# Performance work log

Hardware: AMD Instinct MI355X
Metric: run time of the kernel (lower is better)

The kernel has to match this reference:

```python
import jax, jax.numpy as jnp
import numpy as np

N = 100000
E = 1600000
D_IN = 64
HIDDEN = [64, 64]
D_OUT = 64


def _sage_layer(x, src, dst, Wl, bl, Wr):
    # gather source features, scatter-max into destination nodes
    agg = jax.ops.segment_max(x[src], dst, num_segments=x.shape[0])  # [N, d_in]
    agg = jnp.where(jnp.isfinite(agg), agg, jnp.zeros((), x.dtype))  # isolated nodes -> 0 (PyG fill)
    return agg @ Wl + bl + x @ Wr  # lin_l(aggr) + lin_r(x), bias only on lin_l


def setup_inputs() -> dict:
    key = jax.random.key(0)
    ks = jax.random.split(key, 12)
    x = jax.random.normal(ks[0], (N, D_IN), dtype=jnp.float32)
    edge_index = jax.random.randint(ks[1], (2, E), 0, N, dtype=jnp.int64)
    dims = [D_IN] + HIDDEN + [D_OUT]  # [64, 64, 64, 64]
    inp = {"x": x, "edge_index": edge_index}
    for i in range(3):
        din, dout = dims[i], dims[i + 1]
        s = 1.0 / np.sqrt(din)
        inp[f"Wl{i}"] = jax.random.uniform(ks[2 + 3 * i], (din, dout), jnp.float32, -s, s)
        inp[f"bl{i}"] = jax.random.uniform(ks[3 + 3 * i], (dout,), jnp.float32, -s, s)
        inp[f"Wr{i}"] = jax.random.uniform(ks[4 + 3 * i], (din, dout), jnp.float32, -s, s)
    return inp


def reference(x, edge_index, Wl0, bl0, Wr0, Wl1, bl1, Wr1, Wl2, bl2, Wr2):
    src, dst = edge_index[0], edge_index[1]
    # dropout p=0.0 -> identity; relu after every conv including the last
    h = jax.nn.relu(_sage_layer(x, src, dst, Wl0, bl0, Wr0))
    h = jax.nn.relu(_sage_layer(h, src, dst, Wl1, bl1, Wr1))
    h = jax.nn.relu(_sage_layer(h, src, dst, Wl2, bl2, Wr2))
    return h
```

## Files before the change

### kernel.cpp

```cpp
#include <hip/hip_runtime.h>
#include <math.h>

#define THREADS 256
#define CHUNK 4096
#define SLAB 4096

typedef __attribute__((ext_vector_type(8))) short bf16x8;
typedef __attribute__((ext_vector_type(4))) float f32x4;

__device__ __forceinline__ float bf_lo(unsigned w) { return __uint_as_float(w << 16); }
__device__ __forceinline__ float bf_hi(unsigned w) { return __uint_as_float(w & 0xffff0000u); }
__device__ __forceinline__ unsigned rne(float f) {
    unsigned b = __float_as_uint(f);
    return b + 0x7fffu + ((b >> 16) & 1u);
}

__device__ __forceinline__ int detect64(const int* __restrict__ ei) {
    return ((ei[1] | ei[3] | ei[5] | ei[7] | ei[9] | ei[11]) == 0) ? 1 : 0;
}
__device__ __forceinline__ int get_src(const int* ei, int e, int i, int is64) {
    return is64 ? (int)((const long long*)ei)[i] : ei[i];
}
__device__ __forceinline__ int get_dst(const int* ei, int e, int i, int is64) {
    return is64 ? (int)((const long long*)ei)[e + i] : ei[e + i];
}

__global__ void k_zero_int(int* __restrict__ p, int n) {
    int i = blockIdx.x * blockDim.x + threadIdx.x;
    if (i < n) p[i] = 0;
}

__global__ __launch_bounds__(256) void k_cvtw(const float4* __restrict__ x4, uint2* __restrict__ hb, int n4,
                                              const float* __restrict__ Wl0, const float* __restrict__ Wr0,
                                              const float* __restrict__ Wl1, const float* __restrict__ Wr1,
                                              const float* __restrict__ Wl2, const float* __restrict__ Wr2,
                                              unsigned* __restrict__ wt0, unsigned* __restrict__ wt1,
                                              unsigned* __restrict__ wt2) {
    int i = blockIdx.x * 256 + threadIdx.x;
    if (i < n4) {
        float4 v = x4[i];
        unsigned p0 = (rne(v.x) >> 16) | (rne(v.y) & 0xffff0000u);
        unsigned p1 = (rne(v.z) >> 16) | (rne(v.w) & 0xffff0000u);
        hb[i] = make_uint2(p0, p1);
        return;
    }
    int id = i - n4;
    if (id < 3 * 4096) {
        int layer = id >> 12;
        int r = id & 4095;
        const float* Wl = (layer == 0) ? Wl0 : (layer == 1) ? Wl1 : Wl2;
        const float* Wr = (layer == 0) ? Wr0 : (layer == 1) ? Wr1 : Wr2;
        unsigned* wt = (layer == 0) ? wt0 : (layer == 1) ? wt1 : wt2;
        int nrow = r >> 6;
        int k2 = r & 63;
        const float* W = (k2 < 32) ? Wl : Wr;
        int k = (k2 < 32) ? (k2 * 2) : (k2 * 2 - 64);
        unsigned lo = rne(W[k * 64 + nrow]) >> 16;
        unsigned hi = rne(W[(k + 1) * 64 + nrow]) & 0xffff0000u;
        wt[nrow * 64 + k2] = lo | hi;
    }
}


__global__ __launch_bounds__(256) void k_bscatter(const int* __restrict__ ei, int e,
                                                  int* __restrict__ bucket_cur,
                                                  int* __restrict__ part, int nbuckets) {
    __shared__ int hist[1024];
    __shared__ int basev[1024];
    int t = threadIdx.x;
#pragma unroll
    for (int j = 0; j < 4; j++) hist[t + j * 256] = 0;
    __syncthreads();
    int is64 = detect64(ei);
    int base = blockIdx.x * CHUNK;
    int ds[16], ss[16];
#pragma unroll
    for (int it = 0; it < 16; it++) {
        int i = base + t + it * 256;
        ds[it] = -1;
        ss[it] = 0;
        if (i < e) {
            ds[it] = get_dst(ei, e, i, is64);
            ss[it] = get_src(ei, e, i, is64);
            atomicAdd(&hist[ds[it] >> 7], 1);
        }
    }
    __syncthreads();
#pragma unroll
    for (int j = 0; j < 4; j++) {
        int b = t + j * 256;
        if (b < nbuckets) {
            int c = hist[b];
            if (c) basev[b] = atomicAdd(&bucket_cur[b], c);
        }
    }
    __syncthreads();
#pragma unroll
    for (int it = 0; it < 16; it++) {
        if (ds[it] >= 0) {
            int bk = ds[it] >> 7;
            int pos = atomicAdd(&basev[bk], 1);
            pos = min(pos, SLAB - 1);
            part[bk * SLAB + pos] = (ss[it] << 7) | (ds[it] & 127);
        }
    }
}

__global__ __launch_bounds__(1024) void k_bscan(const int* __restrict__ bucket_cnt, int nbuckets,
                                                int* __restrict__ bucket_ptr,
                                                int* __restrict__ row_ptr, int n, int e) {
    __shared__ int s[1024];
    int t = threadIdx.x;
    int v = (t < nbuckets) ? bucket_cnt[t] : 0;
    s[t] = v;
    __syncthreads();
    for (int off = 1; off < 1024; off <<= 1) {
        int u = (t >= off) ? s[t - off] : 0;
        __syncthreads();
        s[t] += u;
        __syncthreads();
    }
    if (t < nbuckets) bucket_ptr[t] = s[t] - v;
    if (t == 0) {
        bucket_ptr[nbuckets] = e;
        row_ptr[n] = e;
    }
}

__global__ __launch_bounds__(256) void k_bfinal(const int* __restrict__ part,
                                                const int* __restrict__ bucket_ptr,
                                                int* __restrict__ row_ptr,
                                                int* __restrict__ col, int n) {
    __shared__ int deg[128], cur[128], sc[128];
    int b = blockIdx.x, t = threadIdx.x;
    int beg = bucket_ptr[b], end = bucket_ptr[b + 1];
    int cnt = end - beg;
    const int* slab = part + b * SLAB;
    int node0 = b << 7;
    if (t < 128) deg[t] = 0;
    __syncthreads();
    for (int i = t; i < cnt; i += 256) atomicAdd(&deg[slab[i] & 127], 1);
    __syncthreads();
    int v = (t < 128) ? deg[t] : 0;
    if (t < 128) sc[t] = v;
    __syncthreads();
    for (int off = 1; off < 128; off <<= 1) {
        int u = (t < 128 && t >= off) ? sc[t - off] : 0;
        __syncthreads();
        if (t < 128) sc[t] += u;
        __syncthreads();
    }
    if (t < 128) {
        int ex = beg + sc[t] - v;
        if (node0 + t < n) row_ptr[node0 + t] = ex;
        cur[t] = ex;
    }
    __syncthreads();
    for (int i = t; i < cnt; i += 256) {
        int p = slab[i];
        int pos = atomicAdd(&cur[p & 127], 1);
        col[pos] = p >> 7;
    }
}

__global__ __launch_bounds__(512, 8) void k_fused(const unsigned* __restrict__ hin,
                                                  const int* __restrict__ row_ptr,
                                                  const int* __restrict__ col,
                                                  const unsigned* __restrict__ Wt,
                                                  const float* __restrict__ bl,
                                                  float* __restrict__ outf,
                                                  unsigned* __restrict__ outb,
                                                  int n) {
    __shared__ char smem[17408 + 17408 + 256];
    short (*Abuf)[136] = (short(*)[136])smem;
    float (*Cs)[68] = (float(*)[68])smem;
    short (*Wts)[136] = (short(*)[136])(smem + 17408);
    float* bs = (float*)(smem + 34816);

    int t = threadIdx.x;
    int node0 = blockIdx.x * 64;

#pragma unroll
    for (int it = 0; it < 2; it++) {
        int c = t + it * 512;
        int nr = c >> 4, k16 = c & 15;
        uint4 w = *(const uint4*)(Wt + nr * 64 + k16 * 4);
        *(uint4*)&Wts[nr][k16 * 8] = w;
    }
    {
        int row = t >> 3, k8 = t & 7;
        int node = node0 + row;
        uint4 w = make_uint4(0, 0, 0, 0);
        if (node < n) w = *(const uint4*)(hin + (size_t)node * 32 + k8 * 4);
        *(uint4*)&Abuf[row][64 + k8 * 8] = w;
    }
    if (t < 64) bs[t] = bl[t];

    int off = (t & 15) << 1;
#pragma unroll
    for (int pass = 0; pass < 2; pass++) {
        int gl = pass * 32 + (t >> 4);
        int g = node0 + gl;
        float4 m = make_float4(0.f, 0.f, 0.f, 0.f);
        if (g < n) {
            int b = row_ptr[g], e = row_ptr[g + 1];
            if (b < e) {
                m = make_float4(-INFINITY, -INFINITY, -INFINITY, -INFINITY);
                int e1 = e - 1;
                for (int k = b; k < e; k += 16) {
                    int s0 = col[min(k, e1)];
                    int s1 = col[min(k + 1, e1)];
                    int s2 = col[min(k + 2, e1)];
                    int s3 = col[min(k + 3, e1)];
                    int s4 = col[min(k + 4, e1)];
                    int s5 = col[min(k + 5, e1)];
                    int s6 = col[min(k + 6, e1)];
                    int s7 = col[min(k + 7, e1)];
                    uint2 r0 = *(const uint2*)(hin + (unsigned)(s0 * 32 + off));
                    uint2 r1 = *(const uint2*)(hin + (unsigned)(s1 * 32 + off));
                    uint2 r2 = *(const uint2*)(hin + (unsigned)(s2 * 32 + off));
                    uint2 r3 = *(const uint2*)(hin + (unsigned)(s3 * 32 + off));
                    uint2 r4 = *(const uint2*)(hin + (unsigned)(s4 * 32 + off));
                    uint2 r5 = *(const uint2*)(hin + (unsigned)(s5 * 32 + off));
                    uint2 r6 = *(const uint2*)(hin + (unsigned)(s6 * 32 + off));
                    uint2 r7 = *(const uint2*)(hin + (unsigned)(s7 * 32 + off));
                    int u0 = col[min(k + 8, e1)];
                    int u1 = col[min(k + 9, e1)];
                    int u2 = col[min(k + 10, e1)];
                    int u3 = col[min(k + 11, e1)];
                    int u4 = col[min(k + 12, e1)];
                    int u5 = col[min(k + 13, e1)];
                    int u6 = col[min(k + 14, e1)];
                    int u7 = col[min(k + 15, e1)];
                    uint2 q0 = *(const uint2*)(hin + (unsigned)(u0 * 32 + off));
                    uint2 q1 = *(const uint2*)(hin + (unsigned)(u1 * 32 + off));
                    uint2 q2 = *(const uint2*)(hin + (unsigned)(u2 * 32 + off));
                    uint2 q3 = *(const uint2*)(hin + (unsigned)(u3 * 32 + off));
                    uint2 q4 = *(const uint2*)(hin + (unsigned)(u4 * 32 + off));
                    uint2 q5 = *(const uint2*)(hin + (unsigned)(u5 * 32 + off));
                    uint2 q6 = *(const uint2*)(hin + (unsigned)(u6 * 32 + off));
                    uint2 q7 = *(const uint2*)(hin + (unsigned)(u7 * 32 + off));
                    m.x = fmaxf(m.x, fmaxf(fmaxf(fmaxf(bf_lo(r0.x), bf_lo(r1.x)), fmaxf(bf_lo(r2.x), bf_lo(r3.x))),
                                           fmaxf(fmaxf(bf_lo(r4.x), bf_lo(r5.x)), fmaxf(bf_lo(r6.x), bf_lo(r7.x)))));
                    m.y = fmaxf(m.y, fmaxf(fmaxf(fmaxf(bf_hi(r0.x), bf_hi(r1.x)), fmaxf(bf_hi(r2.x), bf_hi(r3.x))),
                                           fmaxf(fmaxf(bf_hi(r4.x), bf_hi(r5.x)), fmaxf(bf_hi(r6.x), bf_hi(r7.x)))));
                    m.z = fmaxf(m.z, fmaxf(fmaxf(fmaxf(bf_lo(r0.y), bf_lo(r1.y)), fmaxf(bf_lo(r2.y), bf_lo(r3.y))),
                                           fmaxf(fmaxf(bf_lo(r4.y), bf_lo(r5.y)), fmaxf(bf_lo(r6.y), bf_lo(r7.y)))));
                    m.w = fmaxf(m.w, fmaxf(fmaxf(fmaxf(bf_hi(r0.y), bf_hi(r1.y)), fmaxf(bf_hi(r2.y), bf_hi(r3.y))),
                                           fmaxf(fmaxf(bf_hi(r4.y), bf_hi(r5.y)), fmaxf(bf_hi(r6.y), bf_hi(r7.y)))));
                    m.x = fmaxf(m.x, fmaxf(fmaxf(fmaxf(bf_lo(q0.x), bf_lo(q1.x)), fmaxf(bf_lo(q2.x), bf_lo(q3.x))),
                                           fmaxf(fmaxf(bf_lo(q4.x), bf_lo(q5.x)), fmaxf(bf_lo(q6.x), bf_lo(q7.x)))));
                    m.y = fmaxf(m.y, fmaxf(fmaxf(fmaxf(bf_hi(q0.x), bf_hi(q1.x)), fmaxf(bf_hi(q2.x), bf_hi(q3.x))),
                                           fmaxf(fmaxf(bf_hi(q4.x), bf_hi(q5.x)), fmaxf(bf_hi(q6.x), bf_hi(q7.x)))));
                    m.z = fmaxf(m.z, fmaxf(fmaxf(fmaxf(bf_lo(q0.y), bf_lo(q1.y)), fmaxf(bf_lo(q2.y), bf_lo(q3.y))),
                                           fmaxf(fmaxf(bf_lo(q4.y), bf_lo(q5.y)), fmaxf(bf_lo(q6.y), bf_lo(q7.y)))));
                    m.w = fmaxf(m.w, fmaxf(fmaxf(fmaxf(bf_hi(q0.y), bf_hi(q1.y)), fmaxf(bf_hi(q2.y), bf_hi(q3.y))),
                                           fmaxf(fmaxf(bf_hi(q4.y), bf_hi(q5.y)), fmaxf(bf_hi(q6.y), bf_hi(q7.y)))));
                }
            }
        }
        unsigned p0 = (__float_as_uint(m.x) >> 16) | (__float_as_uint(m.y) & 0xffff0000u);
        unsigned p1 = (__float_as_uint(m.z) >> 16) | (__float_as_uint(m.w) & 0xffff0000u);
        *(uint2*)&Abuf[gl][(t & 15) * 4] = make_uint2(p0, p1);
    }
    __syncthreads();

    int lane = t & 63;
    int wv = t >> 6;
    int r0 = (wv & 3) * 16;
    int c0 = (wv >> 2) * 32;
    int lr = lane & 15, lk = lane >> 4;

    f32x4 acc0 = {0.f, 0.f, 0.f, 0.f}, acc1 = acc0;
#pragma unroll
    for (int kk = 0; kk < 4; kk++) {
        int ko = kk * 32 + lk * 8;
        bf16x8 a = *(const bf16x8*)&Abuf[r0 + lr][ko];
        bf16x8 b0 = *(const bf16x8*)&Wts[c0 + lr][ko];
        bf16x8 b1 = *(const bf16x8*)&Wts[c0 + 16 + lr][ko];
        acc0 = __builtin_amdgcn_mfma_f32_16x16x32_bf16(a, b0, acc0, 0, 0, 0);
        acc1 = __builtin_amdgcn_mfma_f32_16x16x32_bf16(a, b1, acc1, 0, 0, 0);
    }
    __syncthreads();
#pragma unroll
    for (int reg = 0; reg < 4; reg++) {
        int row = r0 + lk * 4 + reg;
        Cs[row][c0 + lr] = acc0[reg];
        Cs[row][c0 + 16 + lr] = acc1[reg];
    }
    __syncthreads();

#pragma unroll
    for (int it = 0; it < 2; it++) {
        int idx = t + it * 512;
        int row = idx >> 4, qc = idx & 15;
        int node = node0 + row;
        if (node < n) {
            float4 v = *(float4*)&Cs[row][qc * 4];
            float4 bb = *(float4*)&bs[qc * 4];
            float4 o;
            o.x = fmaxf(v.x + bb.x, 0.f);
            o.y = fmaxf(v.y + bb.y, 0.f);
            o.z = fmaxf(v.z + bb.z, 0.f);
            o.w = fmaxf(v.w + bb.w, 0.f);
            if (outf) *(float4*)(outf + (size_t)node * 64 + qc * 4) = o;
            if (outb) {
                unsigned p0 = (rne(o.x) >> 16) | (rne(o.y) & 0xffff0000u);
                unsigned p1 = (rne(o.z) >> 16) | (rne(o.w) & 0xffff0000u);
                *(uint2*)(outb + (size_t)node * 32 + qc * 2) = make_uint2(p0, p1);
            }
        }
    }
}


extern "C" void kernel_launch(void* const* d_in, const int* in_sizes, int n_in,
                              void* d_out, int out_size, void* d_ws, size_t ws_size,
                              hipStream_t stream) {
    const float* x = (const float*)d_in[0];
    const int* ei = (const int*)d_in[1];
    const float* Wl0 = (const float*)d_in[2];
    const float* bl0 = (const float*)d_in[3];
    const float* Wr0 = (const float*)d_in[4];
    const float* Wl1 = (const float*)d_in[5];
    const float* bl1 = (const float*)d_in[6];
    const float* Wr1 = (const float*)d_in[7];
    const float* Wl2 = (const float*)d_in[8];
    const float* bl2 = (const float*)d_in[9];
    const float* Wr2 = (const float*)d_in[10];

    int n = in_sizes[0] / 64;
    int e = in_sizes[1] / 2;
    int nbuckets = (n + 127) >> 7;

    char* p = (char*)d_ws;
    auto alloc = [&](size_t bytes) {
        void* q = (void*)p;
        p += (bytes + 255) & ~(size_t)255;
        return q;
    };
    int* bucket_cur = (int*)alloc((size_t)nbuckets * 4);
    int* bucket_ptr = (int*)alloc(((size_t)nbuckets + 1) * 4);
    int* row_ptr = (int*)alloc(((size_t)n + 1) * 4);
    int* col = (int*)alloc((size_t)e * 4);
    int* part = (int*)alloc((size_t)nbuckets * SLAB * 4);
    unsigned* hb0 = (unsigned*)alloc((size_t)n * 64 * 2);
    unsigned* hb1 = (unsigned*)alloc((size_t)n * 64 * 2);
    unsigned* wt0 = (unsigned*)alloc(64 * 64 * 4);
    unsigned* wt1 = (unsigned*)alloc(64 * 64 * 4);
    unsigned* wt2 = (unsigned*)alloc(64 * 64 * 4);

    float* out = (float*)d_out;

    int gb_chunk = (e + CHUNK - 1) / CHUNK;
    int gb_fused = (n + 63) / 64;
    int n4 = n * 16;
    int gb_cvtw = (n4 + 3 * 4096 + THREADS - 1) / THREADS;

    k_zero_int<<<(nbuckets + THREADS - 1) / THREADS, THREADS, 0, stream>>>(bucket_cur, nbuckets);
    k_bscatter<<<gb_chunk, 256, 0, stream>>>(ei, e, bucket_cur, part, nbuckets);
    k_bscan<<<1, 1024, 0, stream>>>(bucket_cur, nbuckets, bucket_ptr, row_ptr, n, e);
    k_bfinal<<<nbuckets, 256, 0, stream>>>(part, bucket_ptr, row_ptr, col, n);

    k_cvtw<<<gb_cvtw, THREADS, 0, stream>>>((const float4*)x, (uint2*)hb0, n4,
                                            Wl0, Wr0, Wl1, Wr1, Wl2, Wr2, wt0, wt1, wt2);

    k_fused<<<gb_fused, 512, 0, stream>>>(hb0, row_ptr, col, wt0, bl0, (float*)nullptr, hb1, n);
    k_fused<<<gb_fused, 512, 0, stream>>>(hb1, row_ptr, col, wt1, bl1, (float*)nullptr, hb0, n);
    k_fused<<<gb_fused, 512, 0, stream>>>(hb0, row_ptr, col, wt2, bl2, out, (unsigned*)nullptr, n);
}
```

Before: 176.1 us.

## Use order-preserving bf16 encoding with packed u16 max and padded slab CSR

Stores bf16 features in a monotone unsigned encoding so the segment max can use packed v_pk_max_u16 instead of unpacking to fp32 and calling fmaxf. The CSR is rebuilt per bucket slab with each node's degree padded to a multiple of 8 (padding repeats the first neighbour) and column entries pre-scaled to byte offsets, which allows aligned int4 column loads without clamping. The global bucket scan kernel is removed, and row_beg/row_end arrays replace row_ptr. The cost is extra encode/decode work, padded gathers on low-degree nodes, and a larger col buffer.

Result: faster. 157.1 us (-10.8%).

```diff
diff --git a/kernel.cpp b/kernel.cpp
--- a/kernel.cpp
+++ b/kernel.cpp
@@ -8,11 +8,23 @@
 typedef __attribute__((ext_vector_type(8))) short bf16x8;
 typedef __attribute__((ext_vector_type(4))) float f32x4;
 
-__device__ __forceinline__ float bf_lo(unsigned w) { return __uint_as_float(w << 16); }
-__device__ __forceinline__ float bf_hi(unsigned w) { return __uint_as_float(w & 0xffff0000u); }
 __device__ __forceinline__ unsigned rne(float f) {
     unsigned b = __float_as_uint(f);
     return b + 0x7fffu + ((b >> 16) & 1u);
+}
+
+__device__ __forceinline__ unsigned enc_map(unsigned u) {
+    return u ^ (((((u >> 15) & 0x00010001u) * 0xFFFFu)) | 0x80008000u);
+}
+__device__ __forceinline__ unsigned dec_map(unsigned e) {
+    return e ^ ((((((~e) >> 15) & 0x00010001u) * 0xFFFFu)) | 0x80008000u);
+}
+#define ENC_NEG_INF 0x007F007Fu
+
+__device__ __forceinline__ unsigned pkmax(unsigned a, unsigned b) {
+    unsigned d;
+    asm("v_pk_max_u16 %0, %1, %2" : "=v"(d) : "v"(a), "v"(b));
+    return d;
 }
 
 __device__ __forceinline__ int detect64(const int* __restrict__ ei) {
@@ -41,7 +53,7 @@
         float4 v = x4[i];
         unsigned p0 = (rne(v.x) >> 16) | (rne(v.y) & 0xffff0000u);
         unsigned p1 = (rne(v.z) >> 16) | (rne(v.w) & 0xffff0000u);
-        hb[i] = make_uint2(p0, p1);
+        hb[i] = make_uint2(enc_map(p0), enc_map(p1));
         return;
     }
     int id = i - n4;
@@ -106,35 +118,14 @@
     }
 }
 
-__global__ __launch_bounds__(1024) void k_bscan(const int* __restrict__ bucket_cnt, int nbuckets,
-                                                int* __restrict__ bucket_ptr,
-                                                int* __restrict__ row_ptr, int n, int e) {
-    __shared__ int s[1024];
-    int t = threadIdx.x;
-    int v = (t < nbuckets) ? bucket_cnt[t] : 0;
-    s[t] = v;
-    __syncthreads();
-    for (int off = 1; off < 1024; off <<= 1) {
-        int u = (t >= off) ? s[t - off] : 0;
-        __syncthreads();
-        s[t] += u;
-        __syncthreads();
-    }
-    if (t < nbuckets) bucket_ptr[t] = s[t] - v;
-    if (t == 0) {
-        bucket_ptr[nbuckets] = e;
-        row_ptr[n] = e;
-    }
-}
-
 __global__ __launch_bounds__(256) void k_bfinal(const int* __restrict__ part,
-                                                const int* __restrict__ bucket_ptr,
-                                                int* __restrict__ row_ptr,
+                                                const int* __restrict__ bucket_cnt,
+                                                int* __restrict__ row_beg,
+                                                int* __restrict__ row_end,
                                                 int* __restrict__ col, int n) {
     __shared__ int deg[128], cur[128], sc[128];
     int b = blockIdx.x, t = threadIdx.x;
-    int beg = bucket_ptr[b], end = bucket_ptr[b + 1];
-    int cnt = end - beg;
+    int cnt = bucket_cnt[b];
     const int* slab = part + b * SLAB;
     int node0 = b << 7;
     if (t < 128) deg[t] = 0;
@@ -142,7 +133,8 @@
     for (int i = t; i < cnt; i += 256) atomicAdd(&deg[slab[i] & 127], 1);
     __syncthreads();
     int v = (t < 128) ? deg[t] : 0;
-    if (t < 128) sc[t] = v;
+    int dp = (v > 0) ? ((v + 7) & ~7) : 0;
+    if (t < 128) sc[t] = dp;
     __syncthreads();
     for (int off = 1; off < 128; off <<= 1) {
         int u = (t < 128 && t >= off) ? sc[t - off] : 0;
@@ -150,21 +142,33 @@
         if (t < 128) sc[t] += u;
         __syncthreads();
     }
+    int base = b * SLAB;
+    int beg = 0;
     if (t < 128) {
-        int ex = beg + sc[t] - v;
-        if (node0 + t < n) row_ptr[node0 + t] = ex;
-        cur[t] = ex;
+        beg = base + sc[t] - dp;
+        int node = node0 + t;
+        if (node < n) {
+            row_beg[node] = beg;
+            row_end[node] = beg + dp;
+        }
+        cur[t] = beg;
     }
     __syncthreads();
     for (int i = t; i < cnt; i += 256) {
         int p = slab[i];
         int pos = atomicAdd(&cur[p & 127], 1);
-        col[pos] = p >> 7;
+        col[pos] = p & ~127;
+    }
+    __syncthreads();
+    if (t < 128 && v > 0) {
+        int first = col[beg];
+        for (int j = v; j < dp; j++) col[beg + j] = first;
     }
 }
 
 __global__ __launch_bounds__(512, 8) void k_fused(const unsigned* __restrict__ hin,
-                                                  const int* __restrict__ row_ptr,
+                                                  const int* __restrict__ row_beg,
+                                                  const int* __restrict__ row_end,
                                                   const int* __restrict__ col,
                                                   const unsigned* __restrict__ Wt,
                                                   const float* __restrict__ bl,
@@ -191,77 +195,50 @@
         int row = t >> 3, k8 = t & 7;
         int node = node0 + row;
         uint4 w = make_uint4(0, 0, 0, 0);
-        if (node < n) w = *(const uint4*)(hin + (size_t)node * 32 + k8 * 4);
+        if (node < n) {
+            w = *(const uint4*)(hin + (size_t)node * 32 + k8 * 4);
+            w.x = dec_map(w.x);
+            w.y = dec_map(w.y);
+            w.z = dec_map(w.z);
+            w.w = dec_map(w.w);
+        }
         *(uint4*)&Abuf[row][64 + k8 * 8] = w;
     }
     if (t < 64) bs[t] = bl[t];
 
-    int off = (t & 15) << 1;
+    const char* hp = (const char*)hin;
+    int off8 = (t & 15) << 3;
 #pragma unroll
     for (int pass = 0; pass < 2; pass++) {
         int gl = pass * 32 + (t >> 4);
         int g = node0 + gl;
-        float4 m = make_float4(0.f, 0.f, 0.f, 0.f);
+        uint2 res = make_uint2(0u, 0u);
         if (g < n) {
-            int b = row_ptr[g], e = row_ptr[g + 1];
+            int b = row_beg[g], e = row_end[g];
             if (b < e) {
-                m = make_float4(-INFINITY, -INFINITY, -INFINITY, -INFINITY);
-                int e1 = e - 1;
-                for (int k = b; k < e; k += 16) {
-                    int s0 = col[min(k, e1)];
-                    int s1 = col[min(k + 1, e1)];
-                    int s2 = col[min(k + 2, e1)];
-                    int s3 = col[min(k + 3, e1)];
-                    int s4 = col[min(k + 4, e1)];
-                    int s5 = col[min(k + 5, e1)];
-                    int s6 = col[min(k + 6, e1)];
-                    int s7 = col[min(k + 7, e1)];
-                    uint2 r0 = *(const uint2*)(hin + (unsigned)(s0 * 32 + off));
-                    uint2 r1 = *(const uint2*)(hin + (unsigned)(s1 * 32 + off));
-                    uint2 r2 = *(const uint2*)(hin + (unsigned)(s2 * 32 + off));
-                    uint2 r3 = *(const uint2*)(hin + (unsigned)(s3 * 32 + off));
-                    uint2 r4 = *(const uint2*)(hin + (unsigned)(s4 * 32 + off));
-                    uint2 r5 = *(const uint2*)(hin + (unsigned)(s5 * 32 + off));
-                    uint2 r6 = *(const uint2*)(hin + (unsigned)(s6 * 32 + off));
-                    uint2 r7 = *(const uint2*)(hin + (unsigned)(s7 * 32 + off));
-                    int u0 = col[min(k + 8, e1)];
-                    int u1 = col[min(k + 9, e1)];
-                    int u2 = col[min(k + 10, e1)];
-                    int u3 = col[min(k + 11, e1)];
-                    int u4 = col[min(k + 12, e1)];
-                    int u5 = col[min(k + 13, e1)];
-                    int u6 = col[min(k + 14, e1)];
-                    int u7 = col[min(k + 15, e1)];
-                    uint2 q0 = *(const uint2*)(hin + (unsigned)(u0 * 32 + off));
-                    uint2 q1 = *(const uint2*)(hin + (unsigned)(u1 * 32 + off));
-                    uint2 q2 = *(const uint2*)(hin + (unsigned)(u2 * 32 + off));
-                    uint2 q3 = *(const uint2*)(hin + (unsigned)(u3 * 32 + off));
-                    uint2 q4 = *(const uint2*)(hin + (unsigned)(u4 * 32 + off));
-                    uint2 q5 = *(const uint2*)(hin + (unsigned)(u5 * 32 + off));
-                    uint2 q6 = *(const uint2*)(hin + (unsigned)(u6 * 32 + off));
-                    uint2 q7 = *(const uint2*)(hin + (unsigned)(u7 * 32 + off));
-                    m.x = fmaxf(m.x, fmaxf(fmaxf(fmaxf(bf_lo(r0.x), bf_lo(r1.x)), fmaxf(bf_lo(r2.x), bf_lo(r3.x))),
-                                           fmaxf(fmaxf(bf_lo(r4.x), bf_lo(r5.x)), fmaxf(bf_lo(r6.x), bf_lo(r7.x)))));
-                    m.y = fmaxf(m.y, fmaxf(fmaxf(fmaxf(bf_hi(r0.x), bf_hi(r1.x)), fmaxf(bf_hi(r2.x), bf_hi(r3.x))),
-                                           fmaxf(fmaxf(bf_hi(r4.x), bf_hi(r5.x)), fmaxf(bf_hi(r6.x), bf_hi(r7.x)))));
-                    m.z = fmaxf(m.z, fmaxf(fmaxf(fmaxf(bf_lo(r0.y), bf_lo(r1.y)), fmaxf(bf_lo(r2.y), bf_lo(r3.y))),
-                                           fmaxf(fmaxf(bf_lo(r4.y), bf_lo(r5.y)), fmaxf(bf_lo(r6.y), bf_lo(r7.y)))));
-                    m.w = fmaxf(m.w, fmaxf(fmaxf(fmaxf(bf_hi(r0.y), bf_hi(r1.y)), fmaxf(bf_hi(r2.y), bf_hi(r3.y))),
-                                           fmaxf(fmaxf(bf_hi(r4.y), bf_hi(r5.y)), fmaxf(bf_hi(r6.y), bf_hi(r7.y)))));
-                    m.x = fmaxf(m.x, fmaxf(fmaxf(fmaxf(bf_lo(q0.x), bf_lo(q1.x)), fmaxf(bf_lo(q2.x), bf_lo(q3.x))),
-                                           fmaxf(fmaxf(bf_lo(q4.x), bf_lo(q5.x)), fmaxf(bf_lo(q6.x), bf_lo(q7.x)))));
-                    m.y = fmaxf(m.y, fmaxf(fmaxf(fmaxf(bf_hi(q0.x), bf_hi(q1.x)), fmaxf(bf_hi(q2.x), bf_hi(q3.x))),
-                                           fmaxf(fmaxf(bf_hi(q4.x), bf_hi(q5.x)), fmaxf(bf_hi(q6.x), bf_hi(q7.x)))));
-                    m.z = fmaxf(m.z, fmaxf(fmaxf(fmaxf(bf_lo(q0.y), bf_lo(q1.y)), fmaxf(bf_lo(q2.y), bf_lo(q3.y))),
-                                           fmaxf(fmaxf(bf_lo(q4.y), bf_lo(q5.y)), fmaxf(bf_lo(q6.y), bf_lo(q7.y)))));
-                    m.w = fmaxf(m.w, fmaxf(fmaxf(fmaxf(bf_hi(q0.y), bf_hi(q1.y)), fmaxf(bf_hi(q2.y), bf_hi(q3.y))),
-                                           fmaxf(fmaxf(bf_hi(q4.y), bf_hi(q5.y)), fmaxf(bf_hi(q6.y), bf_hi(q7.y)))));
+                unsigned m0 = ENC_NEG_INF, m1 = ENC_NEG_INF;
+                for (int k = b; k < e; k += 8) {
+                    int4 c0 = *(const int4*)(col + k);
+                    int4 c1 = *(const int4*)(col + k + 4);
+                    uint2 r0 = *(const uint2*)(hp + (unsigned)(c0.x + off8));
+                    uint2 r1 = *(const uint2*)(hp + (unsigned)(c0.y + off8));
+                    uint2 r2 = *(const uint2*)(hp + (unsigned)(c0.z + off8));
+                    uint2 r3 = *(const uint2*)(hp + (unsigned)(c0.w + off8));
+                    uint2 r4 = *(const uint2*)(hp + (unsigned)(c1.x + off8));
+                    uint2 r5 = *(const uint2*)(hp + (unsigned)(c1.y + off8));
+                    uint2 r6 = *(const uint2*)(hp + (unsigned)(c1.z + off8));
+                    uint2 r7 = *(const uint2*)(hp + (unsigned)(c1.w + off8));
+                    unsigned a0 = pkmax(pkmax(r0.x, r1.x), pkmax(r2.x, r3.x));
+                    unsigned a1 = pkmax(pkmax(r4.x, r5.x), pkmax(r6.x, r7.x));
+                    unsigned b0 = pkmax(pkmax(r0.y, r1.y), pkmax(r2.y, r3.y));
+                    unsigned b1 = pkmax(pkmax(r4.y, r5.y), pkmax(r6.y, r7.y));
+                    m0 = pkmax(m0, pkmax(a0, a1));
+                    m1 = pkmax(m1, pkmax(b0, b1));
                 }
+                res = make_uint2(dec_map(m0), dec_map(m1));
             }
         }
-        unsigned p0 = (__float_as_uint(m.x) >> 16) | (__float_as_uint(m.y) & 0xffff0000u);
-        unsigned p1 = (__float_as_uint(m.z) >> 16) | (__float_as_uint(m.w) & 0xffff0000u);
-        *(uint2*)&Abuf[gl][(t & 15) * 4] = make_uint2(p0, p1);
+        *(uint2*)&Abuf[gl][(t & 15) * 4] = res;
     }
     __syncthreads();
 
@@ -307,7 +284,7 @@
             if (outb) {
                 unsigned p0 = (rne(o.x) >> 16) | (rne(o.y) & 0xffff0000u);
                 unsigned p1 = (rne(o.z) >> 16) | (rne(o.w) & 0xffff0000u);
-                *(uint2*)(outb + (size_t)node * 32 + qc * 2) = make_uint2(p0, p1);
+                *(uint2*)(outb + (size_t)node * 32 + qc * 2) = make_uint2(enc_map(p0), enc_map(p1));
             }
         }
     }
@@ -340,9 +317,9 @@
         return q;
     };
     int* bucket_cur = (int*)alloc((size_t)nbuckets * 4);
-    int* bucket_ptr = (int*)alloc(((size_t)nbuckets + 1) * 4);
-    int* row_ptr = (int*)alloc(((size_t)n + 1) * 4);
-    int* col = (int*)alloc((size_t)e * 4);
+    int* row_beg = (int*)alloc((size_t)n * 4);
+    int* row_end = (int*)alloc((size_t)n * 4);
+    int* col = (int*)alloc((size_t)nbuckets * SLAB * 4);
     int* part = (int*)alloc((size_t)nbuckets * SLAB * 4);
     unsigned* hb0 = (unsigned*)alloc((size_t)n * 64 * 2);
     unsigned* hb1 = (unsigned*)alloc((size_t)n * 64 * 2);
@@ -359,13 +336,12 @@
 
     k_zero_int<<<(nbuckets + THREADS - 1) / THREADS, THREADS, 0, stream>>>(bucket_cur, nbuckets);
     k_bscatter<<<gb_chunk, 256, 0, stream>>>(ei, e, bucket_cur, part, nbuckets);
-    k_bscan<<<1, 1024, 0, stream>>>(bucket_cur, nbuckets, bucket_ptr, row_ptr, n, e);
-    k_bfinal<<<nbuckets, 256, 0, stream>>>(part, bucket_ptr, row_ptr, col, n);
+    k_bfinal<<<nbuckets, 256, 0, stream>>>(part, bucket_cur, row_beg, row_end, col, n);
 
     k_cvtw<<<gb_cvtw, THREADS, 0, stream>>>((const float4*)x, (uint2*)hb0, n4,
                                             Wl0, Wr0, Wl1, Wr1, Wl2, Wr2, wt0, wt1, wt2);
 
-    k_fused<<<gb_fused, 512, 0, stream>>>(hb0, row_ptr, col, wt0, bl0, (float*)nullptr, hb1, n);
-    k_fused<<<gb_fused, 512, 0, stream>>>(hb1, row_ptr, col, wt1, bl1, (float*)nullptr, hb0, n);
-    k_fused<<<gb_fused, 512, 0, stream>>>(hb0, row_ptr, col, wt2, bl2, out, (unsigned*)nullptr, n);
-}
+    k_fused<<<gb_fused, 512, 0, stream>>>(hb0, row_beg, row_end, col, wt0, bl0, (float*)nullptr, hb1, n);
+    k_fused<<<gb_fused, 512, 0, stream>>>(hb1, row_beg, row_end, col, wt1, bl1, (float*)nullptr, hb0, n);
+    k_fused<<<gb_fused, 512, 0, stream>>>(hb0, row_beg, row_end, col, wt2, bl2, out, (unsigned*)nullptr, n);
+}
```
